# Optimization experiments

Hardware: AMD Instinct MI355X
Metric: run time of the kernel (lower is better)

The kernel has to match this reference:

```python
import jax, jax.numpy as jnp
import numpy as np

STRIDES = (8, 16, 32, 64, 128)
THRESHOLD = 0.5
B, C = 8, 80
HS = (160, 80, 40, 20, 10)


def setup_inputs() -> dict:
    key = jax.random.key(0)
    ks = jax.random.split(key, 3 * len(HS))
    d = {}
    for i, h in enumerate(HS):
        d[f"cls_{i}"] = jax.random.normal(ks[3 * i], (B, C, h, h), jnp.float32)
        d[f"bbox_{i}"] = jax.random.normal(ks[3 * i + 1], (B, 4, h, h), jnp.float32)
        d[f"ctr_{i}"] = jax.random.normal(ks[3 * i + 2], (B, 1, h, h), jnp.float32)
    return d


def _filter_level(cls, bbox, ctr, stride, thr):
    # cls: [B,C,H,W], bbox: [B,4,H,W], ctr: [B,1,H,W] (NCHW, as asserted in source)
    b, c, h, w = cls.shape
    scores = cls.transpose(0, 2, 3, 1).reshape(b, h * w, c)   # [B,HW,C]
    bboxes = bbox.transpose(0, 2, 3, 1).reshape(b, h * w, 4)  # [B,HW,4]
    ctrs = ctr.transpose(0, 2, 3, 1).reshape(b, h * w, 1)     # [B,HW,1]
    # FilterModule keeps locations whose max class score exceeds threshold.
    mask = (jnp.max(scores, axis=-1) > thr)[..., None].astype(scores.dtype)  # [B,HW,1]
    ys, xs = jnp.meshgrid(jnp.arange(h), jnp.arange(w), indexing="ij")
    half = stride // 2
    coord = jnp.stack([xs * stride + half, ys * stride + half], axis=-1)  # [H,W,2]
    coord = coord.reshape(h * w, 2).astype(scores.dtype)
    coord = jnp.broadcast_to(coord, (b, h * w, 2))
    # Static-shape compaction: zero out non-selected locations instead of
    # producing dynamic-length per-image lists (jit-compatible equivalent of
    # the per-image coord/score/bbox/centerness gather).
    return jnp.concatenate(
        [coord * mask, scores * mask, bboxes * mask, ctrs * mask], axis=-1
    )  # [B, HW, 2 + C + 4 + 1]


def reference(cls_0, bbox_0, ctr_0, cls_1, bbox_1, ctr_1, cls_2, bbox_2, ctr_2,
              cls_3, bbox_3, ctr_3, cls_4, bbox_4, ctr_4):
    levels = [
        (cls_0, bbox_0, ctr_0),
        (cls_1, bbox_1, ctr_1),
        (cls_2, bbox_2, ctr_2),
        (cls_3, bbox_3, ctr_3),
        (cls_4, bbox_4, ctr_4),
    ]
    return tuple(
        _filter_level(c, bb, ct, s, THRESHOLD)
        for (c, bb, ct), s in zip(levels, STRIDES)
    )
```

## Files before the change

kernel.cpp:

```cpp
#include <hip/hip_runtime.h>

#define NCH   85
#define TILE  64
#define LS    67
#define OUTCH 87
#define NF4   1392

typedef float f32x4 __attribute__((ext_vector_type(4)));

__global__ __launch_bounds__(256) void fcos_filter_kernel(
    const float* __restrict__ c0, const float* __restrict__ b0, const float* __restrict__ t0,
    const float* __restrict__ c1, const float* __restrict__ b1, const float* __restrict__ t1,
    const float* __restrict__ c2, const float* __restrict__ b2, const float* __restrict__ t2,
    const float* __restrict__ c3, const float* __restrict__ b3, const float* __restrict__ t3,
    const float* __restrict__ c4, const float* __restrict__ b4, const float* __restrict__ t4,
    float* __restrict__ out)
{
    __shared__ float lds[NCH * LS];
    __shared__ float s_flag[TILE];

    const int bid = blockIdx.x;
    const int tid = threadIdx.x;

    const float *cls, *bbx, *ctr;
    int img, tile, HW, W, str, ksh;
    size_t obase;
    if (bid < 3200)      { cls=c0; bbx=b0; ctr=t0; HW=25600; W=160; str=8;   ksh=4; obase=0u;
                           img = bid / 400;          tile = bid - img * 400; }
    else if (bid < 4000) { cls=c1; bbx=b1; ctr=t1; HW=6400;  W=80;  str=16;  ksh=3; obase=17817600u;
                           const int bl = bid - 3200; img = bl / 100; tile = bl - img * 100; }
    else if (bid < 4200) { cls=c2; bbx=b2; ctr=t2; HW=1600;  W=40;  str=32;  ksh=2; obase=22272000u;
                           const int bl = bid - 4000; img = bl / 25;  tile = bl - img * 25; }
    else if (bid < 4256) { cls=c3; bbx=b3; ctr=t3; HW=400;   W=20;  str=64;  ksh=1; obase=23385600u;
                           const int bl = bid - 4200; img = bl / 7;   tile = bl - img * 7; }
    else                 { cls=c4; bbx=b4; ctr=t4; HW=100;   W=10;  str=128; ksh=0; obase=23664000u;
                           const int bl = bid - 4256; img = bl >> 1;  tile = bl & 1; }

    const int p0    = tile * TILE;
    const int valid = min(TILE, HW - p0);

    const int  lane_c = tid >> 4;
    const int  q4     = (tid & 15) << 2;
    const bool qok    = q4 < valid;

    float4 v0, v1, v2, v3, v4, v5;
    float4 fm = make_float4(-1e30f, -1e30f, -1e30f, -1e30f);
    const float* abase = cls + ((size_t)img * 80 + lane_c) * HW + p0 + q4;
    if (qok) {
        v0 = *reinterpret_cast<const float4*>(abase);
        v1 = *reinterpret_cast<const float4*>(abase + (size_t)16 * HW);
        v2 = *reinterpret_cast<const float4*>(abase + (size_t)32 * HW);
        v3 = *reinterpret_cast<const float4*>(abase + (size_t)48 * HW);
        v4 = *reinterpret_cast<const float4*>(abase + (size_t)64 * HW);
        fm.x = fmaxf(fmaxf(fmaxf(v0.x, v1.x), fmaxf(v2.x, v3.x)), v4.x);
        fm.y = fmaxf(fmaxf(fmaxf(v0.y, v1.y), fmaxf(v2.y, v3.y)), v4.y);
        fm.z = fmaxf(fmaxf(fmaxf(v0.z, v1.z), fmaxf(v2.z, v3.z)), v4.z);
        fm.w = fmaxf(fmaxf(fmaxf(v0.w, v1.w), fmaxf(v2.w, v3.w)), v4.w);
    }
    const bool r5 = (tid < 80) && qok;
    if (r5) {
        const float* s5 = (lane_c < 4)
            ? bbx + ((size_t)img * 4 + lane_c) * HW + p0 + q4
            : ctr + (size_t)img * HW + p0 + q4;
        v5 = *reinterpret_cast<const float4*>(s5);
    }

    #define PUT(base_c, V)                                          \
    {   const int a = (base_c + lane_c) * LS + q4;                  \
        lds[a + 0] = V.x; lds[a + 1] = V.y;                         \
        lds[a + 2] = V.z; lds[a + 3] = V.w;                         \
    }
    if (qok) { PUT(0, v0) PUT(16, v1) PUT(32, v2) PUT(48, v3) PUT(64, v4) }
    if (r5)  { PUT(80, v5) }
    #undef PUT

    fm.x = fmaxf(fm.x, __shfl_xor(fm.x, 16));
    fm.y = fmaxf(fm.y, __shfl_xor(fm.y, 16));
    fm.z = fmaxf(fm.z, __shfl_xor(fm.z, 16));
    fm.w = fmaxf(fm.w, __shfl_xor(fm.w, 16));
    fm.x = fmaxf(fm.x, __shfl_xor(fm.x, 32));
    fm.y = fmaxf(fm.y, __shfl_xor(fm.y, 32));
    fm.z = fmaxf(fm.z, __shfl_xor(fm.z, 32));
    fm.w = fmaxf(fm.w, __shfl_xor(fm.w, 32));

    if (tid < TILE) s_flag[tid] = 0.0f;
    __syncthreads();

    if ((tid & 63) < 16) {
        if (fm.x > 0.5f) s_flag[q4 + 0] = 1.0f;
        if (fm.y > 0.5f) s_flag[q4 + 1] = 1.0f;
        if (fm.z > 0.5f) s_flag[q4 + 2] = 1.0f;
        if (fm.w > 0.5f) s_flag[q4 + 3] = 1.0f;
    }
    __syncthreads();

    float* dst = out + obase + ((size_t)img * HW + p0) * OUTCH;
    const int nmax = valid * OUTCH;
    #pragma unroll
    for (int r = 0; r < 6; ++r) {
        const int f4 = tid + 256 * r;
        if (r == 5 && f4 >= NF4) break;
        const int e0 = f4 * 4;
        if (e0 >= nmax) break;
        const int p  = e0 / OUTCH;
        const int ch = e0 - p * OUTCH;
        float vals[4];
        #pragma unroll
        for (int j = 0; j < 4; ++j) {
            int chj = ch + j, pj = p;
            if (chj >= OUTCH) { chj -= OUTCH; pj += 1; }
            const float m = s_flag[pj];
            float val;
            if (chj >= 2) {
                val = lds[(chj - 2) * LS + pj] * m;
            } else {
                const int pg = p0 + pj;
                const int t  = pg >> ksh;
                const int y  = t / 10;
                const int x  = pg - y * W;
                const int coord = (chj == 0) ? x : y;
                val = (float)(coord * str + (str >> 1)) * m;
            }
            vals[j] = val;
        }
        if (e0 + 4 <= nmax) {
            f32x4 o; o.x = vals[0]; o.y = vals[1]; o.z = vals[2]; o.w = vals[3];
            __builtin_nontemporal_store(o, reinterpret_cast<f32x4*>(dst + e0));
        } else {
            #pragma unroll
            for (int j = 0; j < 4; ++j)
                if (e0 + j < nmax) __builtin_nontemporal_store(vals[j], dst + e0 + j);
        }
    }
}

extern "C" void kernel_launch(void* const* d_in, const int* in_sizes, int n_in,
                              void* d_out, int out_size, void* d_ws, size_t ws_size,
                              hipStream_t stream) {
    (void)in_sizes; (void)n_in; (void)out_size; (void)d_ws; (void)ws_size;
    fcos_filter_kernel<<<4272, 256, 0, stream>>>(
        (const float*)d_in[0],  (const float*)d_in[1],  (const float*)d_in[2],
        (const float*)d_in[3],  (const float*)d_in[4],  (const float*)d_in[5],
        (const float*)d_in[6],  (const float*)d_in[7],  (const float*)d_in[8],
        (const float*)d_in[9],  (const float*)d_in[10], (const float*)d_in[11],
        (const float*)d_in[12], (const float*)d_in[13], (const float*)d_in[14],
        (float*)d_out);
}
```

Measured before the change: 35.48 us.

## Process two tiles per block, prefetching the second tile during the first store

Each block now handles two consecutive tiles, halving the grid. The second tile's global loads are issued into registers before the first tile's output is written, so load latency overlaps with the store phase. The output stores also switch from nontemporal to regular stores. This raises register pressure (two sets of six float4 values), which may lower occupancy, and halving the block count reduces parallelism across CUs.

```diff
diff --git a/kernel.cpp b/kernel.cpp
--- a/kernel.cpp
+++ b/kernel.cpp
@@ -1,6 +1,5 @@
 #include <hip/hip_runtime.h>
 
-#define NCH   85
 #define TILE  64
 #define LS    67
 #define OUTCH 87
@@ -9,136 +8,150 @@
 typedef float f32x4 __attribute__((ext_vector_type(4)));
 
 __global__ __launch_bounds__(256) void fcos_filter_kernel(
-    const float* __restrict__ c0, const float* __restrict__ b0, const float* __restrict__ t0,
-    const float* __restrict__ c1, const float* __restrict__ b1, const float* __restrict__ t1,
-    const float* __restrict__ c2, const float* __restrict__ b2, const float* __restrict__ t2,
-    const float* __restrict__ c3, const float* __restrict__ b3, const float* __restrict__ t3,
-    const float* __restrict__ c4, const float* __restrict__ b4, const float* __restrict__ t4,
+    const float* __restrict__ cl0, const float* __restrict__ bb0, const float* __restrict__ ct0,
+    const float* __restrict__ cl1, const float* __restrict__ bb1, const float* __restrict__ ct1,
+    const float* __restrict__ cl2, const float* __restrict__ bb2, const float* __restrict__ ct2,
+    const float* __restrict__ cl3, const float* __restrict__ bb3, const float* __restrict__ ct3,
+    const float* __restrict__ cl4, const float* __restrict__ bb4, const float* __restrict__ ct4,
     float* __restrict__ out)
 {
-    __shared__ float lds[NCH * LS];
+    __shared__ float lds[85 * LS];
     __shared__ float s_flag[TILE];
 
-    const int bid = blockIdx.x;
+    const int P   = blockIdx.x;
     const int tid = threadIdx.x;
 
     const float *cls, *bbx, *ctr;
-    int img, tile, HW, W, str, ksh;
+    int HW, W, str, ksh, iA, tA, iB, tB;
     size_t obase;
-    if (bid < 3200)      { cls=c0; bbx=b0; ctr=t0; HW=25600; W=160; str=8;   ksh=4; obase=0u;
-                           img = bid / 400;          tile = bid - img * 400; }
-    else if (bid < 4000) { cls=c1; bbx=b1; ctr=t1; HW=6400;  W=80;  str=16;  ksh=3; obase=17817600u;
-                           const int bl = bid - 3200; img = bl / 100; tile = bl - img * 100; }
-    else if (bid < 4200) { cls=c2; bbx=b2; ctr=t2; HW=1600;  W=40;  str=32;  ksh=2; obase=22272000u;
-                           const int bl = bid - 4000; img = bl / 25;  tile = bl - img * 25; }
-    else if (bid < 4256) { cls=c3; bbx=b3; ctr=t3; HW=400;   W=20;  str=64;  ksh=1; obase=23385600u;
-                           const int bl = bid - 4200; img = bl / 7;   tile = bl - img * 7; }
-    else                 { cls=c4; bbx=b4; ctr=t4; HW=100;   W=10;  str=128; ksh=0; obase=23664000u;
-                           const int bl = bid - 4256; img = bl >> 1;  tile = bl & 1; }
+    if (P < 1600)      { cls=cl0;bbx=bb0;ctr=ct0;HW=25600;W=160;str=8;  ksh=4;obase=0u;
+        const int a=2*P;        iA=a/400; tA=a-iA*400; const int b=a+1; iB=b/400; tB=b-iB*400; }
+    else if (P < 2000) { cls=cl1;bbx=bb1;ctr=ct1;HW=6400; W=80; str=16; ksh=3;obase=17817600u;
+        const int a=2*(P-1600); iA=a/100; tA=a-iA*100; const int b=a+1; iB=b/100; tB=b-iB*100; }
+    else if (P < 2100) { cls=cl2;bbx=bb2;ctr=ct2;HW=1600; W=40; str=32; ksh=2;obase=22272000u;
+        const int a=2*(P-2000); iA=a/25;  tA=a-iA*25;  const int b=a+1; iB=b/25;  tB=b-iB*25;  }
+    else if (P < 2128) { cls=cl3;bbx=bb3;ctr=ct3;HW=400;  W=20; str=64; ksh=1;obase=23385600u;
+        const int a=2*(P-2100); iA=a/7;   tA=a-iA*7;   const int b=a+1; iB=b/7;   tB=b-iB*7;   }
+    else               { cls=cl4;bbx=bb4;ctr=ct4;HW=100;  W=10; str=128;ksh=0;obase=23664000u;
+        const int a=2*(P-2128); iA=a>>1;  tA=a&1;      const int b=a+1; iB=b>>1;  tB=b&1;      }
 
-    const int p0    = tile * TILE;
-    const int valid = min(TILE, HW - p0);
+    const int pA = tA * TILE, pB = tB * TILE;
+    const int vA = min(TILE, HW - pA), vB = min(TILE, HW - pB);
 
     const int  lane_c = tid >> 4;
     const int  q4     = (tid & 15) << 2;
-    const bool qok    = q4 < valid;
+    const bool okA    = q4 < vA, okB = q4 < vB;
 
-    float4 v0, v1, v2, v3, v4, v5;
-    float4 fm = make_float4(-1e30f, -1e30f, -1e30f, -1e30f);
-    const float* abase = cls + ((size_t)img * 80 + lane_c) * HW + p0 + q4;
-    if (qok) {
-        v0 = *reinterpret_cast<const float4*>(abase);
-        v1 = *reinterpret_cast<const float4*>(abase + (size_t)16 * HW);
-        v2 = *reinterpret_cast<const float4*>(abase + (size_t)32 * HW);
-        v3 = *reinterpret_cast<const float4*>(abase + (size_t)48 * HW);
-        v4 = *reinterpret_cast<const float4*>(abase + (size_t)64 * HW);
-        fm.x = fmaxf(fmaxf(fmaxf(v0.x, v1.x), fmaxf(v2.x, v3.x)), v4.x);
-        fm.y = fmaxf(fmaxf(fmaxf(v0.y, v1.y), fmaxf(v2.y, v3.y)), v4.y);
-        fm.z = fmaxf(fmaxf(fmaxf(v0.z, v1.z), fmaxf(v2.z, v3.z)), v4.z);
-        fm.w = fmaxf(fmaxf(fmaxf(v0.w, v1.w), fmaxf(v2.w, v3.w)), v4.w);
-    }
-    const bool r5 = (tid < 80) && qok;
-    if (r5) {
-        const float* s5 = (lane_c < 4)
-            ? bbx + ((size_t)img * 4 + lane_c) * HW + p0 + q4
-            : ctr + (size_t)img * HW + p0 + q4;
-        v5 = *reinterpret_cast<const float4*>(s5);
-    }
+    auto load_tile = [&](float4 v[6], int img_, int p0_, bool ok_) {
+        if (ok_) {
+            const float* ab = cls + ((size_t)img_ * 80 + lane_c) * HW + p0_ + q4;
+            v[0] = *reinterpret_cast<const float4*>(ab);
+            v[1] = *reinterpret_cast<const float4*>(ab + (size_t)16 * HW);
+            v[2] = *reinterpret_cast<const float4*>(ab + (size_t)32 * HW);
+            v[3] = *reinterpret_cast<const float4*>(ab + (size_t)48 * HW);
+            v[4] = *reinterpret_cast<const float4*>(ab + (size_t)64 * HW);
+            if (tid < 80) {
+                const float* s5 = (lane_c < 4)
+                    ? bbx + ((size_t)img_ * 4 + lane_c) * HW + p0_ + q4
+                    : ctr + (size_t)img_ * HW + p0_ + q4;
+                v[5] = *reinterpret_cast<const float4*>(s5);
+            }
+        }
+    };
 
-    #define PUT(base_c, V)                                          \
-    {   const int a = (base_c + lane_c) * LS + q4;                  \
-        lds[a + 0] = V.x; lds[a + 1] = V.y;                         \
-        lds[a + 2] = V.z; lds[a + 3] = V.w;                         \
-    }
-    if (qok) { PUT(0, v0) PUT(16, v1) PUT(32, v2) PUT(48, v3) PUT(64, v4) }
-    if (r5)  { PUT(80, v5) }
-    #undef PUT
+    auto commit_tile = [&](const float4 v[6], bool ok_) {
+        float4 fm; fm.x = fm.y = fm.z = fm.w = -1e30f;
+        if (ok_) {
+            #pragma unroll
+            for (int k = 0; k < 5; ++k) {
+                const int a_ = (16 * k + lane_c) * LS + q4;
+                lds[a_ + 0] = v[k].x; lds[a_ + 1] = v[k].y;
+                lds[a_ + 2] = v[k].z; lds[a_ + 3] = v[k].w;
+                fm.x = fmaxf(fm.x, v[k].x);
+                fm.y = fmaxf(fm.y, v[k].y);
+                fm.z = fmaxf(fm.z, v[k].z);
+                fm.w = fmaxf(fm.w, v[k].w);
+            }
+            if (tid < 80) {
+                const int a_ = (80 + lane_c) * LS + q4;
+                lds[a_ + 0] = v[5].x; lds[a_ + 1] = v[5].y;
+                lds[a_ + 2] = v[5].z; lds[a_ + 3] = v[5].w;
+            }
+        }
+        fm.x = fmaxf(fm.x, __shfl_xor(fm.x, 16));
+        fm.y = fmaxf(fm.y, __shfl_xor(fm.y, 16));
+        fm.z = fmaxf(fm.z, __shfl_xor(fm.z, 16));
+        fm.w = fmaxf(fm.w, __shfl_xor(fm.w, 16));
+        fm.x = fmaxf(fm.x, __shfl_xor(fm.x, 32));
+        fm.y = fmaxf(fm.y, __shfl_xor(fm.y, 32));
+        fm.z = fmaxf(fm.z, __shfl_xor(fm.z, 32));
+        fm.w = fmaxf(fm.w, __shfl_xor(fm.w, 32));
+        if (tid < TILE) s_flag[tid] = 0.0f;
+        __syncthreads();
+        if ((tid & 63) < 16) {
+            if (fm.x > 0.5f) s_flag[q4 + 0] = 1.0f;
+            if (fm.y > 0.5f) s_flag[q4 + 1] = 1.0f;
+            if (fm.z > 0.5f) s_flag[q4 + 2] = 1.0f;
+            if (fm.w > 0.5f) s_flag[q4 + 3] = 1.0f;
+        }
+        __syncthreads();
+    };
 
-    fm.x = fmaxf(fm.x, __shfl_xor(fm.x, 16));
-    fm.y = fmaxf(fm.y, __shfl_xor(fm.y, 16));
-    fm.z = fmaxf(fm.z, __shfl_xor(fm.z, 16));
-    fm.w = fmaxf(fm.w, __shfl_xor(fm.w, 16));
-    fm.x = fmaxf(fm.x, __shfl_xor(fm.x, 32));
-    fm.y = fmaxf(fm.y, __shfl_xor(fm.y, 32));
-    fm.z = fmaxf(fm.z, __shfl_xor(fm.z, 32));
-    fm.w = fmaxf(fm.w, __shfl_xor(fm.w, 32));
+    auto store_tile = [&](int img_, int p0_, int valid_) {
+        float* dst = out + obase + ((size_t)img_ * HW + p0_) * OUTCH;
+        const int nmax = valid_ * OUTCH;
+        #pragma unroll
+        for (int r = 0; r < 6; ++r) {
+            const int f4 = tid + 256 * r;
+            if (r == 5 && f4 >= NF4) break;
+            const int e0 = f4 * 4;
+            if (e0 >= nmax) break;
+            const int p  = e0 / OUTCH;
+            const int ch = e0 - p * OUTCH;
+            float vals[4];
+            #pragma unroll
+            for (int j = 0; j < 4; ++j) {
+                int chj = ch + j, pj = p;
+                if (chj >= OUTCH) { chj -= OUTCH; pj += 1; }
+                const float m = s_flag[pj];
+                float val;
+                if (chj >= 2) {
+                    val = lds[(chj - 2) * LS + pj] * m;
+                } else {
+                    const int pg = p0_ + pj;
+                    const int tt = pg >> ksh;
+                    const int y  = tt / 10;
+                    const int x  = pg - y * W;
+                    val = (float)(((chj == 0) ? x : y) * str + (str >> 1)) * m;
+                }
+                vals[j] = val;
+            }
+            if (e0 + 4 <= nmax) {
+                f32x4 o; o.x = vals[0]; o.y = vals[1]; o.z = vals[2]; o.w = vals[3];
+                *reinterpret_cast<f32x4*>(dst + e0) = o;
+            } else {
+                #pragma unroll
+                for (int j = 0; j < 4; ++j)
+                    if (e0 + j < nmax) dst[e0 + j] = vals[j];
+            }
+        }
+    };
 
-    if (tid < TILE) s_flag[tid] = 0.0f;
+    float4 va[6], vb[6];
+    load_tile(va, iA, pA, okA);
+    commit_tile(va, okA);
+    load_tile(vb, iB, pB, okB);
+    store_tile(iA, pA, vA);
     __syncthreads();
-
-    if ((tid & 63) < 16) {
-        if (fm.x > 0.5f) s_flag[q4 + 0] = 1.0f;
-        if (fm.y > 0.5f) s_flag[q4 + 1] = 1.0f;
-        if (fm.z > 0.5f) s_flag[q4 + 2] = 1.0f;
-        if (fm.w > 0.5f) s_flag[q4 + 3] = 1.0f;
-    }
-    __syncthreads();
-
-    float* dst = out + obase + ((size_t)img * HW + p0) * OUTCH;
-    const int nmax = valid * OUTCH;
-    #pragma unroll
-    for (int r = 0; r < 6; ++r) {
-        const int f4 = tid + 256 * r;
-        if (r == 5 && f4 >= NF4) break;
-        const int e0 = f4 * 4;
-        if (e0 >= nmax) break;
-        const int p  = e0 / OUTCH;
-        const int ch = e0 - p * OUTCH;
-        float vals[4];
-        #pragma unroll
-        for (int j = 0; j < 4; ++j) {
-            int chj = ch + j, pj = p;
-            if (chj >= OUTCH) { chj -= OUTCH; pj += 1; }
-            const float m = s_flag[pj];
-            float val;
-            if (chj >= 2) {
-                val = lds[(chj - 2) * LS + pj] * m;
-            } else {
-                const int pg = p0 + pj;
-                const int t  = pg >> ksh;
-                const int y  = t / 10;
-                const int x  = pg - y * W;
-                const int coord = (chj == 0) ? x : y;
-                val = (float)(coord * str + (str >> 1)) * m;
-            }
-            vals[j] = val;
-        }
-        if (e0 + 4 <= nmax) {
-            f32x4 o; o.x = vals[0]; o.y = vals[1]; o.z = vals[2]; o.w = vals[3];
-            __builtin_nontemporal_store(o, reinterpret_cast<f32x4*>(dst + e0));
-        } else {
-            #pragma unroll
-            for (int j = 0; j < 4; ++j)
-                if (e0 + j < nmax) __builtin_nontemporal_store(vals[j], dst + e0 + j);
-        }
-    }
+    commit_tile(vb, okB);
+    store_tile(iB, pB, vB);
 }
 
 extern "C" void kernel_launch(void* const* d_in, const int* in_sizes, int n_in,
                               void* d_out, int out_size, void* d_ws, size_t ws_size,
                               hipStream_t stream) {
     (void)in_sizes; (void)n_in; (void)out_size; (void)d_ws; (void)ws_size;
-    fcos_filter_kernel<<<4272, 256, 0, stream>>>(
+    fcos_filter_kernel<<<2136, 256, 0, stream>>>(
         (const float*)d_in[0],  (const float*)d_in[1],  (const float*)d_in[2],
         (const float*)d_in[3],  (const float*)d_in[4],  (const float*)d_in[5],
         (const float*)d_in[6],  (const float*)d_in[7],  (const float*)d_in[8],
```

After: 36.45 us. 1.03x slower.
